# Kernel optimization log

Hardware: AMD Instinct MI355X
Metric: run time of the kernel (lower is better)

## Reference

```python
import jax, jax.numpy as jnp
import numpy as np

N = 100000   # nodes
E = 1600000  # edges (before self-loops)
DIN, DH, DL = 128, 128, 64


def setup_inputs() -> dict:
    key = jax.random.key(0)
    ks = jax.random.split(key, 6)
    feat = jax.random.normal(ks[0], (N, DIN), dtype=jnp.float32)
    src = jax.random.randint(ks[1], (E,), 0, N)
    dst = jax.random.randint(ks[2], (E,), 0, N)

    def glorot(k, i, o):
        return jax.random.normal(k, (i, o), dtype=jnp.float32) * (1.0 / np.sqrt(i))

    return dict(
        feat=feat, src=src, dst=dst,
        W1=glorot(ks[3], DIN, DH), b1=jnp.zeros((DH,), jnp.float32),
        W2=glorot(ks[4], DH, DH), b2=jnp.zeros((DH,), jnp.float32),
        W3=glorot(ks[5], DH, DL), b3=jnp.zeros((DL,), jnp.float32),
    )


def _graph_conv(feat, src, dst, out_isqrt, in_isqrt, W, b):
    # DGL GraphConv, norm='both': scale src by d_out^{-1/2}, sum messages
    # into dst, scale by d_in^{-1/2}, then dense transform.
    h = feat * out_isqrt[:, None]                                   # [N, F]
    agg = jax.ops.segment_sum(h[src], dst, num_segments=N)          # [N, F]
    agg = agg * in_isqrt[:, None]
    return agg @ W + b


def reference(feat, src, dst, W1, b1, W2, b2, W3, b3):
    # dgl.add_self_loop: append (i, i) for every node
    loops = jnp.arange(N, dtype=src.dtype)
    s = jnp.concatenate([src, loops])
    d = jnp.concatenate([dst, loops])

    ones = jnp.ones(s.shape[0], dtype=feat.dtype)
    deg_out = jax.ops.segment_sum(ones, s, num_segments=N)
    deg_in = jax.ops.segment_sum(ones, d, num_segments=N)
    out_isqrt = jax.lax.rsqrt(jnp.maximum(deg_out, 1.0))
    in_isqrt = jax.lax.rsqrt(jnp.maximum(deg_in, 1.0))

    h = jax.nn.relu(_graph_conv(feat, s, d, out_isqrt, in_isqrt, W1, b1))
    h = jax.nn.relu(_graph_conv(h, s, d, out_isqrt, in_isqrt, W2, b2))
    return _graph_conv(h, s, d, out_isqrt, in_isqrt, W3, b3)
```

## Files before the change

### kernel.cpp

```cpp
#include <hip/hip_runtime.h>
#include <hip/hip_fp16.h>

#define NN 100000
#define NE 1600000
#define KDIM 128

#define BSH 8
#define NBKT ((NN + 255) >> BSH)
#define BCAP 6144
#define CHUNK 4096
#define CPAD 16

#define SRC_MASK 0x1FFFFu

typedef _Float16 half8 __attribute__((ext_vector_type(8)));
typedef float f32x4 __attribute__((ext_vector_type(4)));

template <int NOUT>
__device__ inline void packW_body(const float* __restrict__ W, _Float16* __restrict__ Wp,
                                  int blk) {
    constexpr int NT = NOUT / 16;
    int idx = blk * 256 + threadIdx.x;
    if (idx >= 128 * NOUT) return;
    int j = idx & 7;
    int l = (idx >> 3) & 63;
    int rest = idx >> 9;
    int nt = rest % NT;
    int kt = rest / NT;
    int k = kt * 32 + ((l >> 4) & 3) * 8 + j;
    int n = nt * 16 + (l & 15);
    Wp[idx] = (_Float16)W[(size_t)k * NOUT + n];
}

__global__ __launch_bounds__(256) void k_prep(const float* __restrict__ W1,
                                              const float* __restrict__ W2,
                                              const float* __restrict__ W3,
                                              _Float16* __restrict__ Wp1,
                                              _Float16* __restrict__ Wp2,
                                              _Float16* __restrict__ Wp3,
                                              unsigned* __restrict__ cursor_d,
                                              unsigned* __restrict__ cursor_s) {
    int b = blockIdx.x;
    if (b < 64) packW_body<128>(W1, Wp1, b);
    else if (b < 128) packW_body<128>(W2, Wp2, b - 64);
    else if (b < 160) packW_body<64>(W3, Wp3, b - 128);
    else {
        for (int k = threadIdx.x; k < NBKT; k += 256) {
            cursor_d[(size_t)k * CPAD] = (unsigned)k * BCAP;
            cursor_s[(size_t)k * CPAD] = (unsigned)k * BCAP;
        }
    }
}

__global__ __launch_bounds__(256) void k_cvt(const float* __restrict__ f,
                                             __half* __restrict__ o) {
    int i = blockIdx.x * 256 + threadIdx.x;
    if (i < NN * KDIM / 4) {
        float4 v = ((const float4*)f)[i];
        __half2 a = __floats2half2_rn(v.x, v.y);
        __half2 b = __floats2half2_rn(v.z, v.w);
        __half2* dst = (__half2*)o + 2 * (size_t)i;
        dst[0] = a;
        dst[1] = b;
    }
}

__global__ __launch_bounds__(512) void k_part2(const int* __restrict__ src,
                                               const int* __restrict__ dst,
                                               unsigned* __restrict__ cursor_d,
                                               unsigned* __restrict__ cursor_s,
                                               unsigned* __restrict__ part_d,
                                               unsigned char* __restrict__ part_s) {
    __shared__ unsigned histd[NBKT];
    __shared__ unsigned hists[NBKT];
    __shared__ unsigned lofsd[NBKT], lofss[NBKT];
    __shared__ unsigned gbased[NBKT], gbases[NBKT];
    __shared__ unsigned sbuf[512];
    __shared__ unsigned staged[CHUNK];
    __shared__ unsigned short stagebd[CHUNK];
    __shared__ unsigned char stages[CHUNK];
    __shared__ unsigned short stagebs[CHUNK];

    const int e0 = blockIdx.x * CHUNK;
    const int lim = min(CHUNK, NE - e0);
    const int t = threadIdx.x;

    for (int k = t; k < NBKT; k += 512) {
        histd[k] = 0u;
        hists[k] = 0u;
    }
    __syncthreads();

    unsigned es[CHUNK / 512], ed[CHUNK / 512];
    int nmine = 0;
#pragma unroll
    for (int i = 0; i < CHUNK / 512; ++i) {
        int r = t + i * 512;
        if (r < lim) {
            es[i] = (unsigned)src[e0 + r];
            ed[i] = (unsigned)dst[e0 + r];
            atomicAdd(&histd[ed[i] >> BSH], 1u);
            atomicAdd(&hists[es[i] >> BSH], 1u);
            nmine = i + 1;
        }
    }
    __syncthreads();

    unsigned vd = (t < NBKT) ? histd[t] : 0u;
    unsigned vs = (t < NBKT) ? hists[t] : 0u;
    unsigned v = (vd << 16) | vs;
    sbuf[t] = v;
    __syncthreads();
    for (int off = 1; off < 512; off <<= 1) {
        unsigned x = sbuf[t];
        if (t >= off) x += sbuf[t - off];
        __syncthreads();
        sbuf[t] = x;
        __syncthreads();
    }
    if (t < NBKT) {
        unsigned ld = (sbuf[t] >> 16) - vd;
        unsigned ls = (sbuf[t] & 0xFFFFu) - vs;
        lofsd[t] = ld;
        lofss[t] = ls;
        gbased[t] = (vd ? atomicAdd(&cursor_d[(size_t)t * CPAD], vd) : 0u) - ld;
        gbases[t] = (vs ? atomicAdd(&cursor_s[(size_t)t * CPAD], vs) : 0u) - ls;
        histd[t] = 0u;
        hists[t] = 0u;
    }
    __syncthreads();

#pragma unroll
    for (int i = 0; i < CHUNK / 512; ++i) {
        if (i < nmine) {
            unsigned kd = ed[i] >> BSH;
            unsigned pd = lofsd[kd] + atomicAdd(&histd[kd], 1u);
            staged[pd] = es[i] | ((ed[i] & 255u) << 17);
            stagebd[pd] = (unsigned short)kd;
            unsigned ks = es[i] >> BSH;
            unsigned ps = lofss[ks] + atomicAdd(&hists[ks], 1u);
            stages[ps] = (unsigned char)(es[i] & 255u);
            stagebs[ps] = (unsigned short)ks;
        }
    }
    __syncthreads();

    for (int j = t; j < lim; j += 512) {
        unsigned k = stagebd[j];
        unsigned gaddr = gbased[k] + (unsigned)j;
        if (gaddr - k * BCAP < BCAP)
            part_d[gaddr] = staged[j];
        unsigned k2 = stagebs[j];
        unsigned gaddr2 = gbases[k2] + (unsigned)j;
        if (gaddr2 - k2 * BCAP < BCAP)
            part_s[gaddr2] = stages[j];
    }
}

__global__ __launch_bounds__(256) void k_cntin(const unsigned* __restrict__ cursor_d,
                                               const unsigned* __restrict__ cursor_s,
                                               const unsigned* __restrict__ part_d,
                                               const unsigned char* __restrict__ part_s,
                                               unsigned* __restrict__ cnt_in,
                                               float* __restrict__ oi,
                                               float* __restrict__ ii,
                                               unsigned* __restrict__ incl,
                                               unsigned* __restrict__ bsums) {
    __shared__ unsigned c[256];
    __shared__ unsigned c2[256];
    __shared__ unsigned s[256];
    const int b = blockIdx.x;
    const int t = threadIdx.x;
    c[t] = 0u;
    c2[t] = 0u;
    __syncthreads();
    unsigned cntd = min(cursor_d[(size_t)b * CPAD] - (unsigned)b * BCAP, (unsigned)BCAP);
    unsigned cnts = min(cursor_s[(size_t)b * CPAD] - (unsigned)b * BCAP, (unsigned)BCAP);
    const unsigned* ppd = part_d + (size_t)b * BCAP;
    const unsigned char* pps = part_s + (size_t)b * BCAP;
    for (unsigned j = t; j < cntd; j += 256)
        atomicAdd(&c[(ppd[j] >> 17) & 255u], 1u);
    for (unsigned j = t; j < cnts; j += 256)
        atomicAdd(&c2[pps[j]], 1u);
    __syncthreads();
    unsigned v = c[t];
    s[t] = v;
    __syncthreads();
    for (int off = 1; off < 256; off <<= 1) {
        unsigned x = s[t];
        if (t >= off) x += s[t - off];
        __syncthreads();
        s[t] = x;
        __syncthreads();
    }
    int node = (b << BSH) + t;
    if (node < NN) {
        cnt_in[node] = v;
        incl[node] = s[t];
        ii[node] = rsqrtf((float)(v + 1u));
        oi[node] = rsqrtf((float)(c2[t] + 1u));
    }
    if (t == 255) bsums[b] = s[255];
}

__global__ __launch_bounds__(256) void k_place(const unsigned* __restrict__ part_d,
                                               const unsigned* __restrict__ incl,
                                               const unsigned* __restrict__ cnt_in,
                                               const unsigned* __restrict__ bsums,
                                               unsigned* __restrict__ row_start,
                                               unsigned* __restrict__ csr) {
    __shared__ unsigned red[256];
    __shared__ unsigned cur[256];
    __shared__ unsigned stage[BCAP];
    const int b = blockIdx.x;
    const int t = threadIdx.x;
    unsigned ps = 0;
    for (int k = t; k < b; k += 256) ps += bsums[k];
    red[t] = ps;
    __syncthreads();
    for (int off = 128; off > 0; off >>= 1) {
        if (t < off) red[t] += red[t + off];
        __syncthreads();
    }
    const unsigned prefix = red[0];

    int node = (b << BSH) + t;
    unsigned cv = 0, iv = 0;
    if (node < NN) {
        cv = cnt_in[node];
        iv = incl[node];
        row_start[node] = prefix + iv - cv;
    }
    cur[t] = iv - cv;
    __syncthreads();
    unsigned cnt = bsums[b];
    const unsigned* pp = part_d + (size_t)b * BCAP;
    for (unsigned j = t; j < cnt; j += 256) {
        unsigned e = pp[j];
        unsigned p = atomicAdd(&cur[(e >> 17) & 255u], 1u);
        stage[p] = e & SRC_MASK;
    }
    __syncthreads();
    for (unsigned j = t; j < cnt; j += 256)
        csr[prefix + j] = stage[j];
}

template <bool SCALE_SRC>
__global__ __launch_bounds__(256) void k_agg128h(const __half* __restrict__ h,
                                                 const float* __restrict__ oi,
                                                 const float* __restrict__ ii,
                                                 const unsigned* __restrict__ row_start,
                                                 const unsigned* __restrict__ cnt_in,
                                                 const unsigned* __restrict__ csr,
                                                 __half* __restrict__ out) {
    int wid = (int)((blockIdx.x * 256u + threadIdx.x) >> 6);
    int lane = threadIdx.x & 63;
    if (wid >= NN) return;
    const __half2* hv = (const __half2*)h;
    float2 acc;
    {
        float2 v = __half22float2(hv[(size_t)wid * 64 + lane]);
        float sc = SCALE_SRC ? oi[wid] : 1.f;
        acc.x = v.x * sc;
        acc.y = v.y * sc;
    }
    unsigned rs = row_start[wid];
    unsigned nk = cnt_in[wid];
    for (unsigned base = 0; base < nk; base += 64) {
        unsigned m = min(64u, nk - base);
        unsigned myidx = ((unsigned)lane < m) ? csr[rs + base + lane] : 0u;
        unsigned k = 0;
        for (; k + 16 <= m; k += 16) {
            unsigned s[16];
            float sc[16];
            __half2 v[16];
#pragma unroll
            for (int i = 0; i < 16; ++i) {
                s[i] = (unsigned)__builtin_amdgcn_readlane((int)myidx, (int)(k + i));
                v[i] = hv[(size_t)s[i] * 64 + lane];
                if (SCALE_SRC) sc[i] = oi[s[i]];
            }
#pragma unroll
            for (int i = 0; i < 16; ++i) {
                float2 f = __half22float2(v[i]);
                if (SCALE_SRC) {
                    acc.x = fmaf(f.x, sc[i], acc.x);
                    acc.y = fmaf(f.y, sc[i], acc.y);
                } else {
                    acc.x += f.x;
                    acc.y += f.y;
                }
            }
        }
        if (k < m) {
            unsigned s[16];
            float sc[16];
            __half2 v[16];
#pragma unroll
            for (int i = 0; i < 16; ++i) {
                s[i] = (unsigned)__builtin_amdgcn_readlane((int)myidx, (int)(k + i));
                v[i] = hv[(size_t)s[i] * 64 + lane];
                float w = SCALE_SRC ? oi[s[i]] : 1.f;
                sc[i] = (k + i < m) ? w : 0.f;
            }
#pragma unroll
            for (int i = 0; i < 16; ++i) {
                float2 f = __half22float2(v[i]);
                acc.x = fmaf(f.x, sc[i], acc.x);
                acc.y = fmaf(f.y, sc[i], acc.y);
            }
        }
    }
    float si = ii[wid];
    ((__half2*)out)[(size_t)wid * 64 + lane] = __floats2half2_rn(acc.x * si, acc.y * si);
}

__global__ __launch_bounds__(256) void k_agg64h(const __half* __restrict__ t,
                                                const float* __restrict__ ii,
                                                const float* __restrict__ bias,
                                                const unsigned* __restrict__ row_start,
                                                const unsigned* __restrict__ cnt_in,
                                                const unsigned* __restrict__ csr,
                                                float* __restrict__ out) {
    int wid = (int)((blockIdx.x * 256u + threadIdx.x) >> 6);
    int lane = threadIdx.x & 63;
    if (wid >= NN) return;
    float acc = __half2float(t[(size_t)wid * 64 + lane]);
    unsigned rs = row_start[wid];
    unsigned nk = cnt_in[wid];
    for (unsigned base = 0; base < nk; base += 64) {
        unsigned m = min(64u, nk - base);
        unsigned myidx = ((unsigned)lane < m) ? csr[rs + base + lane] : 0u;
        unsigned k = 0;
        for (; k + 16 <= m; k += 16) {
            unsigned s[16];
            __half v[16];
#pragma unroll
            for (int i = 0; i < 16; ++i) {
                s[i] = (unsigned)__builtin_amdgcn_readlane((int)myidx, (int)(k + i));
                v[i] = t[(size_t)s[i] * 64 + lane];
            }
#pragma unroll
            for (int i = 0; i < 16; ++i) acc += __half2float(v[i]);
        }
        if (k < m) {
            unsigned s[16];
            float sc[16];
            __half v[16];
#pragma unroll
            for (int i = 0; i < 16; ++i) {
                s[i] = (unsigned)__builtin_amdgcn_readlane((int)myidx, (int)(k + i));
                v[i] = t[(size_t)s[i] * 64 + lane];
                sc[i] = (k + i < m) ? 1.f : 0.f;
            }
#pragma unroll
            for (int i = 0; i < 16; ++i) acc = fmaf(__half2float(v[i]), sc[i], acc);
        }
    }
    out[(size_t)wid * 64 + lane] = acc * ii[wid] + bias[lane];
}

template <int NOUT, bool RELU, bool OSCALE, bool BIAS, bool O32, bool O16>
__global__ __launch_bounds__(256) void k_gemmf(const _Float16* __restrict__ A,
                                               const _Float16* __restrict__ Wp,
                                               const float* __restrict__ bias,
                                               const float* __restrict__ oscale,
                                               float* __restrict__ Y32,
                                               _Float16* __restrict__ Y16) {
    constexpr int NT = NOUT / 16;
    const int w = threadIdx.x >> 6;
    const int l = threadIdx.x & 63;
    const int r0 = blockIdx.x * 128 + w * 32;
    int arow0 = r0 + (l & 15);
    int arow1 = arow0 + 16;
    if (arow0 >= NN) arow0 = NN - 1;
    if (arow1 >= NN) arow1 = NN - 1;
    const half8* Ap0 = (const half8*)(A + (size_t)arow0 * 128) + (l >> 4);
    const half8* Ap1 = (const half8*)(A + (size_t)arow1 * 128) + (l >> 4);
    const half8* Bp = (const half8*)Wp + l;

    f32x4 acc0[NT], acc1[NT];
#pragma unroll
    for (int n = 0; n < NT; ++n) {
        acc0[n] = {0.f, 0.f, 0.f, 0.f};
        acc1[n] = {0.f, 0.f, 0.f, 0.f};
    }

#pragma unroll
    for (int kt = 0; kt < 4; ++kt) {
        half8 a0 = Ap0[kt * 4];
        half8 a1 = Ap1[kt * 4];
#pragma unroll
        for (int n = 0; n < NT; ++n) {
            half8 b = Bp[(kt * NT + n) * 64];
            acc0[n] = __builtin_amdgcn_mfma_f32_16x16x32_f16(a0, b, acc0[n], 0, 0, 0);
            acc1[n] = __builtin_amdgcn_mfma_f32_16x16x32_f16(a1, b, acc1[n], 0, 0, 0);
        }
    }

    const int col = l & 15;
#pragma unroll
    for (int half = 0; half < 2; ++half) {
        const int rbase = r0 + half * 16 + (l >> 4) * 4;
        f32x4* acc = half ? acc1 : acc0;
#pragma unroll
        for (int j = 0; j < 4; ++j) {
            int row = rbase + j;
            if (row >= NN) continue;
            float os = OSCALE ? oscale[row] : 1.f;
#pragma unroll
            for (int n = 0; n < NT; ++n) {
                float v = acc[n][j];
                if (BIAS) v += bias[n * 16 + col];
                if (RELU) v = fmaxf(v, 0.f);
                v *= os;
                if (O32) Y32[(size_t)row * NOUT + n * 16 + col] = v;
                if (O16) Y16[(size_t)row * NOUT + n * 16 + col] = (_Float16)v;
            }
        }
    }
}

extern "C" void kernel_launch(void* const* d_in, const int* in_sizes, int n_in,
                              void* d_out, int out_size, void* d_ws, size_t ws_size,
                              hipStream_t stream) {
    const float* feat = (const float*)d_in[0];
    const int* src = (const int*)d_in[1];
    const int* dst = (const int*)d_in[2];
    const float* W1 = (const float*)d_in[3];
    const float* b1 = (const float*)d_in[4];
    const float* W2 = (const float*)d_in[5];
    const float* b2 = (const float*)d_in[6];
    const float* W3 = (const float*)d_in[7];
    const float* b3 = (const float*)d_in[8];
    float* out = (float*)d_out;

    char* p = (char*)d_ws;
    auto take = [&](size_t bytes) {
        char* q = p;
        p += (bytes + 255) & ~(size_t)255;
        return q;
    };
    unsigned* cnt_in = (unsigned*)take((size_t)NN * 4);
    float* oi = (float*)take((size_t)NN * 4);
    float* ii = (float*)take((size_t)NN * 4);
    unsigned* incl = (unsigned*)take((size_t)NN * 4);
    unsigned* bsums = (unsigned*)take(512 * 4);
    unsigned* row_start = (unsigned*)take((size_t)NN * 4);
    unsigned* cursor_d = (unsigned*)take((size_t)NBKT * CPAD * 4);
    unsigned* cursor_s = (unsigned*)take((size_t)NBKT * CPAD * 4);
    unsigned* csr = (unsigned*)take((size_t)NE * 4);
    unsigned char* part_s = (unsigned char*)take((size_t)NBKT * BCAP);
    __half* feat16 = (__half*)take((size_t)NN * KDIM * 2);
    __half* H16 = (__half*)take((size_t)NN * KDIM * 2);
    __half* G16 = (__half*)take((size_t)NN * KDIM * 2);
    _Float16* Wp1 = (_Float16*)take((size_t)128 * 128 * 2);
    _Float16* Wp2 = (_Float16*)take((size_t)128 * 128 * 2);
    _Float16* Wp3 = (_Float16*)take((size_t)128 * 64 * 2);
    char* regionB = take((size_t)NN * 64 * 2 > (size_t)NBKT * BCAP * 4
                             ? (size_t)NN * 64 * 2
                             : (size_t)NBKT * BCAP * 4);
    unsigned* part_d = (unsigned*)regionB;
    __half* T16 = (__half*)regionB;

    k_prep<<<161, 256, 0, stream>>>(W1, W2, W3, Wp1, Wp2, Wp3, cursor_d, cursor_s);
    k_cvt<<<(NN * KDIM / 4 + 255) / 256, 256, 0, stream>>>(feat, feat16);
    k_part2<<<(NE + CHUNK - 1) / CHUNK, 512, 0, stream>>>(src, dst, cursor_d, cursor_s,
                                                          part_d, part_s);
    k_cntin<<<NBKT, 256, 0, stream>>>(cursor_d, cursor_s, part_d, part_s, cnt_in, oi, ii,
                                      incl, bsums);
    k_place<<<NBKT, 256, 0, stream>>>(part_d, incl, cnt_in, bsums, row_start, csr);

    const int AGG_BLOCKS = (NN + 3) / 4;
    const int GEMM_BLOCKS = (NN + 127) / 128;

    k_agg128h<true><<<AGG_BLOCKS, 256, 0, stream>>>(feat16, oi, ii, row_start, cnt_in, csr, G16);
    k_gemmf<128, true, true, true, false, true>
        <<<GEMM_BLOCKS, 256, 0, stream>>>((const _Float16*)G16, Wp1, b1, oi, nullptr, (_Float16*)H16);
    k_agg128h<false><<<AGG_BLOCKS, 256, 0, stream>>>(H16, oi, ii, row_start, cnt_in, csr, G16);
    k_gemmf<128, true, true, true, false, true>
        <<<GEMM_BLOCKS, 256, 0, stream>>>((const _Float16*)G16, Wp2, b2, oi, nullptr, (_Float16*)H16);
    k_gemmf<64, false, false, false, false, true>
        <<<GEMM_BLOCKS, 256, 0, stream>>>((const _Float16*)H16, Wp3, nullptr, nullptr, nullptr, (_Float16*)T16);
    k_agg64h<<<AGG_BLOCKS, 256, 0, stream>>>(T16, ii, b3, row_start, cnt_in, csr, out);
}
```

Measured before the change: 291.6 us.

## Fuse aggregation with MFMA GEMM per layer and merge CSR build kernels

Each of the first two layers now runs its neighbour aggregation and dense transform in one kernel. Every wave aggregates 16 rows into shared memory and then multiplies them by the packed weights with MFMA, so the G16 intermediate no longer makes a round trip through global memory and one launch per layer is dropped. The count and place kernels are merged into one, with each block computing its prefix from the bucket cursors directly. The feature conversion kernel now handles 8 floats per thread. The risk is lower occupancy in the fused kernel, since each block covers 64 rows with serial per-wave aggregation and uses extra shared memory.

After: 327.8 us. +12.4%, slower.

```diff
diff --git a/kernel.cpp b/kernel.cpp
--- a/kernel.cpp
+++ b/kernel.cpp
@@ -55,13 +55,15 @@
 __global__ __launch_bounds__(256) void k_cvt(const float* __restrict__ f,
                                              __half* __restrict__ o) {
     int i = blockIdx.x * 256 + threadIdx.x;
-    if (i < NN * KDIM / 4) {
-        float4 v = ((const float4*)f)[i];
-        __half2 a = __floats2half2_rn(v.x, v.y);
-        __half2 b = __floats2half2_rn(v.z, v.w);
-        __half2* dst = (__half2*)o + 2 * (size_t)i;
-        dst[0] = a;
-        dst[1] = b;
+    if (i < NN * KDIM / 8) {
+        const float4* f4 = (const float4*)f + 2 * (size_t)i;
+        float4 a = f4[0], b = f4[1];
+        __half2 h0 = __floats2half2_rn(a.x, a.y);
+        __half2 h1 = __floats2half2_rn(a.z, a.w);
+        __half2 h2 = __floats2half2_rn(b.x, b.y);
+        __half2 h3 = __floats2half2_rn(b.z, b.w);
+        __half2 hh[4] = {h0, h1, h2, h3};
+        *((uint4*)o + i) = *(uint4*)hh;
     }
 }
 
@@ -157,23 +159,37 @@
     }
 }
 
-__global__ __launch_bounds__(256) void k_cntin(const unsigned* __restrict__ cursor_d,
+__global__ __launch_bounds__(256) void k_build(const unsigned* __restrict__ cursor_d,
                                                const unsigned* __restrict__ cursor_s,
                                                const unsigned* __restrict__ part_d,
                                                const unsigned char* __restrict__ part_s,
                                                unsigned* __restrict__ cnt_in,
                                                float* __restrict__ oi,
                                                float* __restrict__ ii,
-                                               unsigned* __restrict__ incl,
-                                               unsigned* __restrict__ bsums) {
+                                               unsigned* __restrict__ row_start,
+                                               unsigned* __restrict__ csr) {
     __shared__ unsigned c[256];
     __shared__ unsigned c2[256];
     __shared__ unsigned s[256];
+    __shared__ unsigned red[256];
+    __shared__ unsigned cur[256];
+    __shared__ unsigned stage[BCAP];
     const int b = blockIdx.x;
     const int t = threadIdx.x;
+
+    unsigned ps = 0;
+    for (int k = t; k < b; k += 256)
+        ps += min(cursor_d[(size_t)k * CPAD] - (unsigned)k * BCAP, (unsigned)BCAP);
+    red[t] = ps;
     c[t] = 0u;
     c2[t] = 0u;
     __syncthreads();
+    for (int off = 128; off > 0; off >>= 1) {
+        if (t < off) red[t] += red[t + off];
+        __syncthreads();
+    }
+    const unsigned prefix = red[0];
+
     unsigned cntd = min(cursor_d[(size_t)b * CPAD] - (unsigned)b * BCAP, (unsigned)BCAP);
     unsigned cnts = min(cursor_s[(size_t)b * CPAD] - (unsigned)b * BCAP, (unsigned)BCAP);
     const unsigned* ppd = part_d + (size_t)b * BCAP;
@@ -183,6 +199,7 @@
     for (unsigned j = t; j < cnts; j += 256)
         atomicAdd(&c2[pps[j]], 1u);
     __syncthreads();
+
     unsigned v = c[t];
     s[t] = v;
     __syncthreads();
@@ -196,123 +213,131 @@
     int node = (b << BSH) + t;
     if (node < NN) {
         cnt_in[node] = v;
-        incl[node] = s[t];
         ii[node] = rsqrtf((float)(v + 1u));
         oi[node] = rsqrtf((float)(c2[t] + 1u));
-    }
-    if (t == 255) bsums[b] = s[255];
-}
-
-__global__ __launch_bounds__(256) void k_place(const unsigned* __restrict__ part_d,
-                                               const unsigned* __restrict__ incl,
-                                               const unsigned* __restrict__ cnt_in,
-                                               const unsigned* __restrict__ bsums,
-                                               unsigned* __restrict__ row_start,
-                                               unsigned* __restrict__ csr) {
-    __shared__ unsigned red[256];
-    __shared__ unsigned cur[256];
-    __shared__ unsigned stage[BCAP];
-    const int b = blockIdx.x;
-    const int t = threadIdx.x;
-    unsigned ps = 0;
-    for (int k = t; k < b; k += 256) ps += bsums[k];
-    red[t] = ps;
-    __syncthreads();
-    for (int off = 128; off > 0; off >>= 1) {
-        if (t < off) red[t] += red[t + off];
-        __syncthreads();
-    }
-    const unsigned prefix = red[0];
-
-    int node = (b << BSH) + t;
-    unsigned cv = 0, iv = 0;
-    if (node < NN) {
-        cv = cnt_in[node];
-        iv = incl[node];
-        row_start[node] = prefix + iv - cv;
-    }
-    cur[t] = iv - cv;
-    __syncthreads();
-    unsigned cnt = bsums[b];
-    const unsigned* pp = part_d + (size_t)b * BCAP;
-    for (unsigned j = t; j < cnt; j += 256) {
-        unsigned e = pp[j];
+        row_start[node] = prefix + s[t] - v;
+    }
+    cur[t] = s[t] - v;
+    __syncthreads();
+
+    for (unsigned j = t; j < cntd; j += 256) {
+        unsigned e = ppd[j];
         unsigned p = atomicAdd(&cur[(e >> 17) & 255u], 1u);
         stage[p] = e & SRC_MASK;
     }
     __syncthreads();
-    for (unsigned j = t; j < cnt; j += 256)
+    for (unsigned j = t; j < cntd; j += 256)
         csr[prefix + j] = stage[j];
 }
 
 template <bool SCALE_SRC>
-__global__ __launch_bounds__(256) void k_agg128h(const __half* __restrict__ h,
-                                                 const float* __restrict__ oi,
-                                                 const float* __restrict__ ii,
-                                                 const unsigned* __restrict__ row_start,
-                                                 const unsigned* __restrict__ cnt_in,
-                                                 const unsigned* __restrict__ csr,
-                                                 __half* __restrict__ out) {
-    int wid = (int)((blockIdx.x * 256u + threadIdx.x) >> 6);
-    int lane = threadIdx.x & 63;
-    if (wid >= NN) return;
+__global__ __launch_bounds__(256) void k_aggemm(const __half* __restrict__ h,
+                                                const float* __restrict__ oi,
+                                                const float* __restrict__ ii,
+                                                const unsigned* __restrict__ row_start,
+                                                const unsigned* __restrict__ cnt_in,
+                                                const unsigned* __restrict__ csr,
+                                                const _Float16* __restrict__ Wp,
+                                                const float* __restrict__ bias,
+                                                _Float16* __restrict__ Y16) {
+    constexpr int NT = 8;
+    __shared__ _Float16 As[4][16][136];
+    const int w = threadIdx.x >> 6;
+    const int lane = threadIdx.x & 63;
+    const int r0 = blockIdx.x * 64 + w * 16;
     const __half2* hv = (const __half2*)h;
-    float2 acc;
-    {
-        float2 v = __half22float2(hv[(size_t)wid * 64 + lane]);
-        float sc = SCALE_SRC ? oi[wid] : 1.f;
-        acc.x = v.x * sc;
-        acc.y = v.y * sc;
-    }
-    unsigned rs = row_start[wid];
-    unsigned nk = cnt_in[wid];
-    for (unsigned base = 0; base < nk; base += 64) {
-        unsigned m = min(64u, nk - base);
-        unsigned myidx = ((unsigned)lane < m) ? csr[rs + base + lane] : 0u;
-        unsigned k = 0;
-        for (; k + 16 <= m; k += 16) {
-            unsigned s[16];
-            float sc[16];
-            __half2 v[16];
-#pragma unroll
-            for (int i = 0; i < 16; ++i) {
-                s[i] = (unsigned)__builtin_amdgcn_readlane((int)myidx, (int)(k + i));
-                v[i] = hv[(size_t)s[i] * 64 + lane];
-                if (SCALE_SRC) sc[i] = oi[s[i]];
-            }
-#pragma unroll
-            for (int i = 0; i < 16; ++i) {
-                float2 f = __half22float2(v[i]);
-                if (SCALE_SRC) {
-                    acc.x = fmaf(f.x, sc[i], acc.x);
-                    acc.y = fmaf(f.y, sc[i], acc.y);
-                } else {
-                    acc.x += f.x;
-                    acc.y += f.y;
+
+    for (int i = 0; i < 16; ++i) {
+        int wid = r0 + i;
+        if (wid >= NN) break;
+        float2 acc;
+        {
+            float2 vv = __half22float2(hv[(size_t)wid * 64 + lane]);
+            float sc = SCALE_SRC ? oi[wid] : 1.f;
+            acc.x = vv.x * sc;
+            acc.y = vv.y * sc;
+        }
+        unsigned rs = row_start[wid];
+        unsigned nk = cnt_in[wid];
+        for (unsigned base = 0; base < nk; base += 64) {
+            unsigned m = min(64u, nk - base);
+            unsigned myidx = ((unsigned)lane < m) ? csr[rs + base + lane] : 0u;
+            unsigned k = 0;
+            for (; k + 16 <= m; k += 16) {
+                unsigned sidx[16];
+                float sc[16];
+                __half2 vv[16];
+#pragma unroll
+                for (int q = 0; q < 16; ++q) {
+                    sidx[q] = (unsigned)__builtin_amdgcn_readlane((int)myidx, (int)(k + q));
+                    vv[q] = hv[(size_t)sidx[q] * 64 + lane];
+                    if (SCALE_SRC) sc[q] = oi[sidx[q]];
+                }
+#pragma unroll
+                for (int q = 0; q < 16; ++q) {
+                    float2 f = __half22float2(vv[q]);
+                    if (SCALE_SRC) {
+                        acc.x = fmaf(f.x, sc[q], acc.x);
+                        acc.y = fmaf(f.y, sc[q], acc.y);
+                    } else {
+                        acc.x += f.x;
+                        acc.y += f.y;
+                    }
                 }
             }
-        }
-        if (k < m) {
-            unsigned s[16];
-            float sc[16];
-            __half2 v[16];
-#pragma unroll
-            for (int i = 0; i < 16; ++i) {
-                s[i] = (unsigned)__builtin_amdgcn_readlane((int)myidx, (int)(k + i));
-                v[i] = hv[(size_t)s[i] * 64 + lane];
-                float w = SCALE_SRC ? oi[s[i]] : 1.f;
-                sc[i] = (k + i < m) ? w : 0.f;
+            if (k < m) {
+                unsigned sidx[16];
+                float sc[16];
+                __half2 vv[16];
+#pragma unroll
+                for (int q = 0; q < 16; ++q) {
+                    sidx[q] = (unsigned)__builtin_amdgcn_readlane((int)myidx, (int)(k + q));
+                    vv[q] = hv[(size_t)sidx[q] * 64 + lane];
+                    float wq = SCALE_SRC ? oi[sidx[q]] : 1.f;
+                    sc[q] = (k + q < m) ? wq : 0.f;
+                }
+#pragma unroll
+                for (int q = 0; q < 16; ++q) {
+                    float2 f = __half22float2(vv[q]);
+                    acc.x = fmaf(f.x, sc[q], acc.x);
+                    acc.y = fmaf(f.y, sc[q], acc.y);
+                }
             }
-#pragma unroll
-            for (int i = 0; i < 16; ++i) {
-                float2 f = __half22float2(v[i]);
-                acc.x = fmaf(f.x, sc[i], acc.x);
-                acc.y = fmaf(f.y, sc[i], acc.y);
-            }
-        }
-    }
-    float si = ii[wid];
-    ((__half2*)out)[(size_t)wid * 64 + lane] = __floats2half2_rn(acc.x * si, acc.y * si);
+        }
+        float si = ii[wid];
+        *(__half2*)&As[w][i][lane * 2] = __floats2half2_rn(acc.x * si, acc.y * si);
+    }
+
+    const half8* Bp = (const half8*)Wp + lane;
+    f32x4 acc[NT];
+#pragma unroll
+    for (int n = 0; n < NT; ++n) acc[n] = {0.f, 0.f, 0.f, 0.f};
+    const int fr = lane & 15;
+    const int fg = lane >> 4;
+#pragma unroll
+    for (int kt = 0; kt < 4; ++kt) {
+        half8 a = *(const half8*)&As[w][fr][kt * 32 + fg * 8];
+#pragma unroll
+        for (int n = 0; n < NT; ++n) {
+            half8 b = Bp[(kt * NT + n) * 64];
+            acc[n] = __builtin_amdgcn_mfma_f32_16x16x32_f16(a, b, acc[n], 0, 0, 0);
+        }
+    }
+
+    const int col = lane & 15;
+    const int rbase = r0 + (lane >> 4) * 4;
+#pragma unroll
+    for (int j = 0; j < 4; ++j) {
+        int row = rbase + j;
+        if (row >= NN) continue;
+        float os = oi[row];
+#pragma unroll
+        for (int n = 0; n < NT; ++n) {
+            float vv = acc[n][j] + bias[n * 16 + col];
+            vv = fmaxf(vv, 0.f);
+            Y16[(size_t)row * 128 + n * 16 + col] = (_Float16)(vv * os);
+        }
+    }
 }
 
 __global__ __launch_bounds__(256) void k_agg64h(const __half* __restrict__ t,
@@ -360,12 +385,9 @@
     out[(size_t)wid * 64 + lane] = acc * ii[wid] + bias[lane];
 }
 
-template <int NOUT, bool RELU, bool OSCALE, bool BIAS, bool O32, bool O16>
+template <int NOUT>
 __global__ __launch_bounds__(256) void k_gemmf(const _Float16* __restrict__ A,
                                                const _Float16* __restrict__ Wp,
-                                               const float* __restrict__ bias,
-                                               const float* __restrict__ oscale,
-                                               float* __restrict__ Y32,
                                                _Float16* __restrict__ Y16) {
     constexpr int NT = NOUT / 16;
     const int w = threadIdx.x >> 6;
@@ -407,16 +429,9 @@
         for (int j = 0; j < 4; ++j) {
             int row = rbase + j;
             if (row >= NN) continue;
-            float os = OSCALE ? oscale[row] : 1.f;
-#pragma unroll
-            for (int n = 0; n < NT; ++n) {
-                float v = acc[n][j];
-                if (BIAS) v += bias[n * 16 + col];
-                if (RELU) v = fmaxf(v, 0.f);
-                v *= os;
-                if (O32) Y32[(size_t)row * NOUT + n * 16 + col] = v;
-                if (O16) Y16[(size_t)row * NOUT + n * 16 + col] = (_Float16)v;
-            }
+#pragma unroll
+            for (int n = 0; n < NT; ++n)
+                Y16[(size_t)row * NOUT + n * 16 + col] = (_Float16)acc[n][j];
         }
     }
 }
@@ -444,8 +459,6 @@
     unsigned* cnt_in = (unsigned*)take((size_t)NN * 4);
     float* oi = (float*)take((size_t)NN * 4);
     float* ii = (float*)take((size_t)NN * 4);
-    unsigned* incl = (unsigned*)take((size_t)NN * 4);
-    unsigned* bsums = (unsigned*)take(512 * 4);
     unsigned* row_start = (unsigned*)take((size_t)NN * 4);
     unsigned* cursor_d = (unsigned*)take((size_t)NBKT * CPAD * 4);
     unsigned* cursor_s = (unsigned*)take((size_t)NBKT * CPAD * 4);
@@ -464,23 +477,20 @@
     __half* T16 = (__half*)regionB;
 
     k_prep<<<161, 256, 0, stream>>>(W1, W2, W3, Wp1, Wp2, Wp3, cursor_d, cursor_s);
-    k_cvt<<<(NN * KDIM / 4 + 255) / 256, 256, 0, stream>>>(feat, feat16);
+    k_cvt<<<(NN * KDIM / 8 + 255) / 256, 256, 0, stream>>>(feat, feat16);
     k_part2<<<(NE + CHUNK - 1) / CHUNK, 512, 0, stream>>>(src, dst, cursor_d, cursor_s,
                                                           part_d, part_s);
-    k_cntin<<<NBKT, 256, 0, stream>>>(cursor_d, cursor_s, part_d, part_s, cnt_in, oi, ii,
-                                      incl, bsums);
-    k_place<<<NBKT, 256, 0, stream>>>(part_d, incl, cnt_in, bsums, row_start, csr);
-
+    k_build<<<NBKT, 256, 0, stream>>>(cursor_d, cursor_s, part_d, part_s, cnt_in, oi, ii,
+                                      row_start, csr);
+
+    const int FUSED_BLOCKS = (NN + 63) / 64;
     const int AGG_BLOCKS = (NN + 3) / 4;
     const int GEMM_BLOCKS = (NN + 127) / 128;
 
-    k_agg128h<true><<<AGG_BLOCKS, 256, 0, stream>>>(feat16, oi, ii, row_start, cnt_in, csr, G16);
-    k_gemmf<128, true, true, true, false, true>
-        <<<GEMM_BLOCKS, 256, 0, stream>>>((const _Float16*)G16, Wp1, b1, oi, nullptr, (_Float16*)H16);
-    k_agg128h<false><<<AGG_BLOCKS, 256, 0, stream>>>(H16, oi, ii, row_start, cnt_in, csr, G16);
-    k_gemmf<128, true, true, true, false, true>
-        <<<GEMM_BLOCKS, 256, 0, stream>>>((const _Float16*)G16, Wp2, b2, oi, nullptr, (_Float16*)H16);
-    k_gemmf<64, false, false, false, false, true>
-        <<<GEMM_BLOCKS, 256, 0, stream>>>((const _Float16*)H16, Wp3, nullptr, nullptr, nullptr, (_Float16*)T16);
+    k_aggemm<true><<<FUSED_BLOCKS, 256, 0, stream>>>(feat16, oi, ii, row_start, cnt_in,
+                                                     csr, Wp1, b1, (_Float16*)H16);
+    k_aggemm<false><<<FUSED_BLOCKS, 256, 0, stream>>>(H16, oi, ii, row_start, cnt_in,
+                                                      csr, Wp2, b2, (_Float16*)G16);
+    k_gemmf<64><<<GEMM_BLOCKS, 256, 0, stream>>>((const _Float16*)G16, Wp3, (_Float16*)T16);
     k_agg64h<<<AGG_BLOCKS, 256, 0, stream>>>(T16, ii, b3, row_start, cnt_in, csr, out);
 }
```
